# Performance work log

Measured on AMD Instinct MI355X. Metric: run time of the kernel, lower is better.

The kernel has to match this reference:

```python
import jax, jax.numpy as jnp
import numpy as np


def setup_inputs() -> dict:
    key = jax.random.key(0)
    ks = jax.random.split(key, 5)
    B, D, W = 8, 768, 128
    scale = 1.0 / np.sqrt(D)
    return {
        "x": jax.random.normal(ks[0], (B, D, W, W), dtype=jnp.float32),
        "in_proj_w": jax.random.normal(ks[1], (3 * D, D), dtype=jnp.float32) * scale,
        "in_proj_b": jax.random.normal(ks[2], (3 * D,), dtype=jnp.float32) * 0.01,
        "out_w": jax.random.normal(ks[3], (D, D), dtype=jnp.float32) * scale,
        "out_b": jax.random.normal(ks[4], (D,), dtype=jnp.float32) * 0.01,
        "num_heads": 12,
        "num_tokens": 8,
    }


def reference(x, in_proj_w, in_proj_b, out_w, out_b, num_heads, num_tokens):
    B, D, Wd, Hd = x.shape
    nt = num_tokens
    gs = Hd // nt            # grid (block) size
    T = nt * nt              # number of blocks / queries
    S = gs * gs              # k/v tokens per block
    h = num_heads
    hd = D // h

    # ---- query: adaptive avg pool to (nt, nt), flatten, permute -> (B, T, D)
    q = x.reshape(B, D, nt, gs, nt, gs).mean(axis=(3, 5))      # (B, D, nt, nt)
    q = q.reshape(B, D, T).transpose(0, 2, 1)                   # (B, T, D)

    # ---- key/value: faithful reproduction of unfold + view(x.size()) + reshape
    # torch: kv_perm (B,W,H,D) -> unfold -> (B, nt, nt, D, gs, gs) contiguous,
    # then reinterpreted flat as (B, W*H, D) (scrambles channel/pixel layout).
    t = x.transpose(0, 2, 3, 1)                                 # (B, W, H, D)
    t = t.reshape(B, nt, gs, nt, gs, D).transpose(0, 1, 3, 5, 2, 4)  # (B,nt,nt,D,gs,gs)
    kv = t.reshape(B, T, S, D)                                  # chunked into T blocks of S tokens

    # ---- in-projections (torch MultiheadAttention packed weights)
    Wq, Wk, Wv = in_proj_w[:D], in_proj_w[D:2 * D], in_proj_w[2 * D:]
    bq, bk, bv = in_proj_b[:D], in_proj_b[D:2 * D], in_proj_b[2 * D:]
    qp = (q @ Wq.T + bq).reshape(B, T, h, hd)                   # (B, T, h, hd)
    kp = (kv @ Wk.T + bk).reshape(B, T, S, h, hd)               # (B, T, S, h, hd)
    vp = (kv @ Wv.T + bv).reshape(B, T, S, h, hd)

    # ---- block-local single-query attention, batched over all T blocks
    scores = jnp.einsum("bthd,btshd->bths", qp, kp) / np.sqrt(hd)  # (B, T, h, S)
    attn = jax.nn.softmax(scores, axis=-1)
    ctx = jnp.einsum("bths,btshd->bthd", attn, vp).reshape(B, T, D)

    # ---- out projection
    return ctx @ out_w.T + out_b                                # (B, T, D)
```

## Files before the change

kernel.cpp:

```cpp
#include <hip/hip_runtime.h>
#include <hip/hip_bf16.h>

#define D_ 768
#define W_ 128
#define T_ 64
#define S_ 256
#define H_ 12
#define HH_ 6
#define BT_ 512

__device__ __forceinline__ unsigned short f2bf(float f) {
  unsigned u = __float_as_uint(f);
  u = (u + 0x7FFFu + ((u >> 16) & 1u)) >> 16;
  return (unsigned short)u;
}
__device__ __forceinline__ float bfu(unsigned s) {
  return __uint_as_float(s << 16);
}

__global__ __launch_bounds__(384) void k_pack(const float* __restrict__ x,
                                              unsigned short* __restrict__ packed,
                                              float* __restrict__ q) {
  const int blk  = blockIdx.x;
  const int cc   = blk & 15;
  const int tjp  = (blk >> 4) & 3;
  const int ti   = (blk >> 6) & 7;
  const int b    = blk >> 9;
  const int tid  = threadIdx.x;
  const int c8   = tid & 7;
  const int ch   = tid >> 3;
  const int btl  = c8 >> 2;
  const int btg0 = b*64 + ti*8 + tjp*2;
  const int ch0  = cc * 48;

  __shared__ unsigned short tile[48][2][260];
  __shared__ float poolsc[48][2];

  const float* xcol = x + (size_t)b*D_*16384 + (size_t)(ch0 + ch)*16384
                        + (16*ti)*128 + 32*tjp + c8*4;

  float psum = 0.f;
  #pragma unroll
  for (int r = 0; r < 16; ++r) {
    const float4 v = *(const float4*)(xcol + r*128);
    const int px = r*16 + (c8 & 3)*4;
    unsigned lo = (unsigned)f2bf(v.x) | ((unsigned)f2bf(v.y) << 16);
    unsigned hi = (unsigned)f2bf(v.z) | ((unsigned)f2bf(v.w) << 16);
    *(uint2*)&tile[ch][btl][px] = make_uint2(lo, hi);
    psum += (v.x + v.y) + (v.z + v.w);
  }
  psum += __shfl_xor(psum, 1);
  psum += __shfl_xor(psum, 2);
  if ((c8 & 3) == 0) poolsc[ch][btl] = psum;
  __syncthreads();

  for (int ii = tid; ii < 512; ii += 384) {
    const int bl = ii >> 8, p = ii & 255;
    unsigned short* pbt = packed + ((size_t)(btg0 + bl)*16 + cc)*D_*16;
    #pragma unroll
    for (int c = 0; c < 3; ++c) {
      unsigned u[8];
      #pragma unroll
      for (int k2 = 0; k2 < 8; ++k2) {
        const unsigned a  = tile[3*(2*k2)     + c][bl][p];
        const unsigned b2 = tile[3*(2*k2 + 1) + c][bl][p];
        u[k2] = a | (b2 << 16);
      }
      unsigned short* dst = pbt + (size_t)(c*256 + p)*16;
      *(uint4*)(dst)     = make_uint4(u[0], u[1], u[2], u[3]);
      *(uint4*)(dst + 8) = make_uint4(u[4], u[5], u[6], u[7]);
    }
  }
  if (tid < 96) {
    const int ch2 = tid >> 1, bl = tid & 1;
    q[(size_t)(btg0 + bl)*D_ + ch0 + ch2] = poolsc[ch2][bl] * (1.0f/256.0f);
  }
}

__global__ __launch_bounds__(256) void k_qp(const float* __restrict__ q,
                                            const float* __restrict__ ipw,
                                            const float* __restrict__ ipb,
                                            float* __restrict__ qp) {
  const int jt = blockIdx.x >> 6;
  const int bt0 = (blockIdx.x & 63) * 8;
  const int tid = threadIdx.x;
  const float* Wr = ipw + (size_t)jt*64*D_;
  __shared__ float wt[64][65];
  __shared__ float at[8][65];
  const int i = tid & 63, qw = tid >> 6;
  float acc[2] = {0,0};
  for (int dc = 0; dc < D_; dc += 64) {
    #pragma unroll
    for (int k = 0; k < 4; ++k) {
      const int idx = k*256 + tid;
      const int r = idx >> 4, c4 = idx & 15;
      *(float4*)&wt[r][c4*4] = *(const float4*)(Wr + (size_t)r*D_ + dc + c4*4);
    }
    if (tid < 128) {
      const int r = tid >> 4, c4 = tid & 15;
      *(float4*)&at[r][c4*4] = *(const float4*)(q + (size_t)(bt0 + r)*D_ + dc + c4*4);
    }
    __syncthreads();
    #pragma unroll
    for (int dd = 0; dd < 64; ++dd) {
      const float wv = wt[i][dd];
      #pragma unroll
      for (int k = 0; k < 2; ++k)
        acc[k] += at[qw + k*4][dd] * wv;
    }
    __syncthreads();
  }
  const float bqv = ipb[jt*64 + i];
  #pragma unroll
  for (int k = 0; k < 2; ++k)
    qp[(size_t)(bt0 + qw + k*4)*D_ + jt*64 + i] = acc[k] + bqv;
}

__global__ __launch_bounds__(256) void k_fold(const float* __restrict__ qp,
                                              const float* __restrict__ ipw,
                                              unsigned short* __restrict__ qkout) {
  const int btc = blockIdx.x & 15;
  const int nt  = blockIdx.x >> 4;
  const int h   = nt / 12;
  const int ddc = (nt % 12) * 64;
  const int bt0 = btc * 32;
  const int tid = threadIdx.x;
  __shared__ float qpl[32][68];
  __shared__ float wkl[64][68];
  #pragma unroll
  for (int k = 0; k < 2; ++k) {
    const int idx = k*256 + tid;
    const int r = idx >> 4, c4 = idx & 15;
    *(float4*)&qpl[r][c4*4] = *(const float4*)(qp + (size_t)(bt0 + r)*D_ + h*64 + c4*4);
  }
  #pragma unroll
  for (int k = 0; k < 4; ++k) {
    const int idx = k*256 + tid;
    const int r = idx >> 4, c4 = idx & 15;
    *(float4*)&wkl[r][c4*4] = *(const float4*)(ipw + (size_t)(D_ + h*64 + r)*D_ + ddc + c4*4);
  }
  __syncthreads();
  const int i = tid & 63, qw = tid >> 6;
  float acc[8] = {0,0,0,0,0,0,0,0};
  #pragma unroll 8
  for (int kk = 0; kk < 64; ++kk) {
    const float w = wkl[kk][i];
    #pragma unroll
    for (int k = 0; k < 8; ++k)
      acc[k] += qpl[qw + k*4][kk] * w;
  }
  #pragma unroll
  for (int k = 0; k < 8; ++k)
    qkout[((size_t)(bt0 + qw + k*4)*H_ + h)*D_ + ddc + i] = f2bf(acc[k] * 0.125f);
}

__global__ __launch_bounds__(256) void k_attn3(const unsigned short* __restrict__ packed,
                                               const unsigned short* __restrict__ qkin,
                                               unsigned short* __restrict__ wout) {
  const int bt = blockIdx.x >> 1;
  const int hg = blockIdx.x & 1;
  const int tid = threadIdx.x;
  const int wv = tid >> 6, lane = tid & 63;
  __shared__ float pool_lds[HH_ * D_];
  __shared__ float sc[HH_][S_];

  {
    const uint4* src = (const uint4*)(qkin + ((size_t)bt*H_ + hg*HH_)*D_);
    #pragma unroll
    for (int k = 0; k < 3; ++k) {
      const int idx = k*256 + tid;
      if (idx < 576) {
        const uint4 v = src[idx];
        float* d = pool_lds + idx*8;
        d[0] = bfu(v.x & 0xFFFFu); d[1] = bfu(v.x >> 16);
        d[2] = bfu(v.y & 0xFFFFu); d[3] = bfu(v.y >> 16);
        d[4] = bfu(v.z & 0xFFFFu); d[5] = bfu(v.z >> 16);
        d[6] = bfu(v.w & 0xFFFFu); d[7] = bfu(v.w >> 16);
      }
    }
  }
  __syncthreads();

  float acc[HH_][4];
  #pragma unroll
  for (int h = 0; h < HH_; ++h)
    #pragma unroll
    for (int j = 0; j < 4; ++j) acc[h][j] = 0.f;

  {
    const unsigned short* pb = packed + ((size_t)bt*16 + (lane >> 2))*D_*16 + (lane & 3)*4;
    const int d0 = wv * 192;
    short4 pv[4];
    #pragma unroll
    for (int dd = 0; dd < 4; ++dd)
      pv[dd] = *(const short4*)(pb + (size_t)(d0 + dd)*16);
    #pragma unroll 2
    for (int d4 = 0; d4 < 48; ++d4) {
      const int d = d0 + d4*4;
      short4 nx[4];
      if (d4 < 47) {
        #pragma unroll
        for (int dd = 0; dd < 4; ++dd)
          nx[dd] = *(const short4*)(pb + (size_t)(d + 4 + dd)*16);
      }
      float f[4][4];
      #pragma unroll
      for (int dd = 0; dd < 4; ++dd) {
        f[dd][0] = bfu((unsigned)(unsigned short)pv[dd].x);
        f[dd][1] = bfu((unsigned)(unsigned short)pv[dd].y);
        f[dd][2] = bfu((unsigned)(unsigned short)pv[dd].z);
        f[dd][3] = bfu((unsigned)(unsigned short)pv[dd].w);
      }
      #pragma unroll
      for (int h = 0; h < HH_; ++h) {
        const float4 qv = *(const float4*)&pool_lds[h*D_ + d];
        #pragma unroll
        for (int j = 0; j < 4; ++j)
          acc[h][j] += qv.x*f[0][j] + qv.y*f[1][j] + qv.z*f[2][j] + qv.w*f[3][j];
      }
      #pragma unroll
      for (int dd = 0; dd < 4; ++dd) pv[dd] = nx[dd];
    }
  }
  __syncthreads();

  if (wv == 0) {
    #pragma unroll
    for (int h = 0; h < HH_; ++h)
      *(float4*)&sc[h][lane*4] = make_float4(acc[h][0], acc[h][1], acc[h][2], acc[h][3]);
  } else {
    float* dstp = pool_lds + (size_t)(wv - 1)*(HH_*S_);
    #pragma unroll
    for (int h = 0; h < HH_; ++h)
      *(float4*)&dstp[h*S_ + lane*4] = make_float4(acc[h][0], acc[h][1], acc[h][2], acc[h][3]);
  }
  __syncthreads();
  #pragma unroll
  for (int h = 0; h < HH_; ++h)
    sc[h][tid] += pool_lds[0*(HH_*S_) + h*S_ + tid]
                + pool_lds[1*(HH_*S_) + h*S_ + tid]
                + pool_lds[2*(HH_*S_) + h*S_ + tid];
  __syncthreads();

  if (wv < 3) {
    #pragma unroll
    for (int hh = 0; hh < 2; ++hh) {
      const int h = wv*2 + hh;
      float4 v = *(const float4*)(&sc[h][lane*4]);
      float m = fmaxf(fmaxf(v.x, v.y), fmaxf(v.z, v.w));
      #pragma unroll
      for (int off = 32; off > 0; off >>= 1) m = fmaxf(m, __shfl_xor(m, off));
      const float e0 = __expf(v.x - m), e1 = __expf(v.y - m),
                  e2 = __expf(v.z - m), e3 = __expf(v.w - m);
      float ss = (e0+e1)+(e2+e3);
      #pragma unroll
      for (int off = 32; off > 0; off >>= 1) ss += __shfl_xor(ss, off);
      const float inv = 1.0f / ss;
      *(float4*)(&sc[h][lane*4]) = make_float4(e0*inv, e1*inv, e2*inv, e3*inv);
    }
  }
  __syncthreads();

  float wacc[HH_][3];
  #pragma unroll
  for (int h = 0; h < HH_; ++h) { wacc[h][0]=0.f; wacc[h][1]=0.f; wacc[h][2]=0.f; }
  const unsigned short* prow = packed + (size_t)bt*16*D_*16;
  uint4 pv3[3];
  #pragma unroll
  for (int c = 0; c < 3; ++c)
    pv3[c] = *(const uint4*)(prow + ((size_t)0*D_ + c*256 + tid)*16);
  #pragma unroll 2
  for (int s8 = 0; s8 < 32; ++s8) {
    uint4 nx3[3];
    if (s8 < 31) {
      const int t = s8 + 1;
      #pragma unroll
      for (int c = 0; c < 3; ++c)
        nx3[c] = *(const uint4*)(prow + ((size_t)(t >> 1)*D_ + c*256 + tid)*16 + (t & 1)*8);
    }
    float f[3][8];
    #pragma unroll
    for (int c = 0; c < 3; ++c) {
      f[c][0] = bfu(pv3[c].x & 0xFFFFu); f[c][1] = bfu(pv3[c].x >> 16);
      f[c][2] = bfu(pv3[c].y & 0xFFFFu); f[c][3] = bfu(pv3[c].y >> 16);
      f[c][4] = bfu(pv3[c].z & 0xFFFFu); f[c][5] = bfu(pv3[c].z >> 16);
      f[c][6] = bfu(pv3[c].w & 0xFFFFu); f[c][7] = bfu(pv3[c].w >> 16);
    }
    #pragma unroll
    for (int h = 0; h < HH_; ++h) {
      const float4 a0 = *(const float4*)&sc[h][s8*8];
      const float4 a1 = *(const float4*)&sc[h][s8*8 + 4];
      #pragma unroll
      for (int c = 0; c < 3; ++c)
        wacc[h][c] += a0.x*f[c][0] + a0.y*f[c][1] + a0.z*f[c][2] + a0.w*f[c][3]
                    + a1.x*f[c][4] + a1.y*f[c][5] + a1.z*f[c][6] + a1.w*f[c][7];
    }
    #pragma unroll
    for (int c = 0; c < 3; ++c) pv3[c] = nx3[c];
  }
  unsigned short* wp = wout + ((size_t)bt*H_ + hg*HH_)*D_;
  #pragma unroll
  for (int h = 0; h < HH_; ++h)
    #pragma unroll
    for (int c = 0; c < 3; ++c)
      wp[h*D_ + c*256 + tid] = f2bf(wacc[h][c]);
}

__global__ __launch_bounds__(256) void k_ctx(const unsigned short* __restrict__ wbuf,
                                             const float* __restrict__ ipw,
                                             const float* __restrict__ ipb,
                                             float* __restrict__ ctx) {
  const int h = blockIdx.x >> 6;
  const int bt0 = (blockIdx.x & 63) * 8;
  const int tid = threadIdx.x;
  const float* Wv = ipw + (size_t)2*D_*D_ + (size_t)h*64*D_;
  __shared__ float wt[64][65];
  __shared__ float at[8][65];
  const int i = tid & 63, qw = tid >> 6;
  float acc[2] = {0,0};
  for (int dc = 0; dc < D_; dc += 64) {
    #pragma unroll
    for (int k = 0; k < 4; ++k) {
      const int idx = k*256 + tid;
      const int r = idx >> 4, c4 = idx & 15;
      *(float4*)&wt[r][c4*4] = *(const float4*)(Wv + (size_t)r*D_ + dc + c4*4);
    }
    if (tid < 128) {
      const int r = tid >> 4, c4 = tid & 15;
      const uint2 v = *(const uint2*)(wbuf + ((size_t)(bt0 + r)*H_ + h)*D_ + dc + c4*4);
      at[r][c4*4 + 0] = bfu(v.x & 0xFFFFu);
      at[r][c4*4 + 1] = bfu(v.x >> 16);
      at[r][c4*4 + 2] = bfu(v.y & 0xFFFFu);
      at[r][c4*4 + 3] = bfu(v.y >> 16);
    }
    __syncthreads();
    #pragma unroll
    for (int dd = 0; dd < 64; ++dd) {
      const float wv = wt[i][dd];
      #pragma unroll
      for (int k = 0; k < 2; ++k)
        acc[k] += at[qw + k*4][dd] * wv;
    }
    __syncthreads();
  }
  const float bvv = ipb[2*D_ + h*64 + i];
  #pragma unroll
  for (int k = 0; k < 2; ++k)
    ctx[(size_t)(bt0 + qw + k*4)*D_ + h*64 + i] = acc[k] + bvv;
}

__global__ __launch_bounds__(256) void k_out(const float* __restrict__ ctx,
                                             const float* __restrict__ ow,
                                             const float* __restrict__ ob,
                                             float* __restrict__ out) {
  const int jt = blockIdx.x >> 6;
  const int bt0 = (blockIdx.x & 63) * 8;
  const int tid = threadIdx.x;
  const float* Wr = ow + (size_t)jt*64*D_;
  __shared__ float wt[64][65];
  __shared__ float at[8][65];
  const int i = tid & 63, qw = tid >> 6;
  float acc[2] = {0,0};
  for (int dc = 0; dc < D_; dc += 64) {
    #pragma unroll
    for (int k = 0; k < 4; ++k) {
      const int idx = k*256 + tid;
      const int r = idx >> 4, c4 = idx & 15;
      *(float4*)&wt[r][c4*4] = *(const float4*)(Wr + (size_t)r*D_ + dc + c4*4);
    }
    if (tid < 128) {
      const int r = tid >> 4, c4 = tid & 15;
      *(float4*)&at[r][c4*4] = *(const float4*)(ctx + (size_t)(bt0 + r)*D_ + dc + c4*4);
    }
    __syncthreads();
    #pragma unroll
    for (int dd = 0; dd < 64; ++dd) {
      const float wv = wt[i][dd];
      #pragma unroll
      for (int k = 0; k < 2; ++k)
        acc[k] += at[qw + k*4][dd] * wv;
    }
    __syncthreads();
  }
  const float obv = ob[jt*64 + i];
  #pragma unroll
  for (int k = 0; k < 2; ++k)
    out[(size_t)(bt0 + qw + k*4)*D_ + jt*64 + i] = acc[k] + obv;
}

__global__ __launch_bounds__(256) void k_q(const float* __restrict__ x, float* __restrict__ q) {
  const int bd = blockIdx.x;
  const int tid = threadIdx.x;
  const float4* xp = (const float4*)(x + (size_t)bd * (W_*W_));
  float acc[8] = {0,0,0,0,0,0,0,0};
  #pragma unroll
  for (int k = 0; k < 16; ++k) {
    float4 v = xp[k*256 + tid];
    acc[k>>1] += (v.x + v.y) + (v.z + v.w);
  }
  __shared__ float part[256][9];
  #pragma unroll
  for (int i = 0; i < 8; ++i) part[tid][i] = acc[i];
  __syncthreads();
  if (tid < 64) {
    const int ti = tid >> 3, tj = tid & 7;
    float s = 0.f;
    #pragma unroll
    for (int m = 0; m < 8; ++m)
      #pragma unroll
      for (int n = 0; n < 4; ++n)
        s += part[m*32 + tj*4 + n][ti];
    const int b = bd / D_, d = bd - b*D_;
    q[(size_t)(b*T_ + tid)*D_ + d] = s * (1.0f/256.0f);
  }
}

__global__ __launch_bounds__(256) void k_attn(const float* __restrict__ x,
                                              const unsigned short* __restrict__ qkin,
                                              unsigned short* __restrict__ wout) {
  const int bt = blockIdx.x;
  const int b = bt >> 6, t = bt & 63;
  const int ti = t >> 3, tj = t & 7;
  const int tid = threadIdx.x;
  __shared__ float qkl[H_*D_];
  __shared__ float sc[H_][S_];
  const float* xb = x + (size_t)b*D_*W_*W_ + ti*16*W_ + tj*16;
  {
    const uint4* src = (const uint4*)(qkin + (size_t)bt*H_*D_);
    #pragma unroll
    for (int k = 0; k < 5; ++k) {
      const int idx = k*256 + tid;
      if (idx < 1152) {
        const uint4 v = src[idx];
        float* d = qkl + idx*8;
        d[0] = bfu(v.x & 0xFFFFu); d[1] = bfu(v.x >> 16);
        d[2] = bfu(v.y & 0xFFFFu); d[3] = bfu(v.y >> 16);
        d[4] = bfu(v.z & 0xFFFFu); d[5] = bfu(v.z >> 16);
        d[6] = bfu(v.w & 0xFFFFu); d[7] = bfu(v.w >> 16);
      }
    }
  }
  __syncthreads();
  float acc[H_];
  #pragma unroll
  for (int h = 0; h < H_; ++h) acc[h] = 0.f;
  #pragma unroll
  for (int c = 0; c < 3; ++c) {
    const float* chp = xb + (size_t)(3*tid + c)*(W_*W_);
    for (int blk = 0; blk < 8; ++blk) {
      float4 v[8];
      #pragma unroll
      for (int u = 0; u < 8; ++u) {
        const int pg = blk*8 + u;
        v[u] = *(const float4*)(chp + (pg>>2)*W_ + (pg&3)*4);
      }
      const int dbase = c*256 + blk*32;
      #pragma unroll
      for (int h = 0; h < H_; ++h) {
        const float4* qh = (const float4*)(qkl + h*D_ + dbase);
        float s0 = 0.f;
        #pragma unroll
        for (int u = 0; u < 8; ++u) {
          const float4 qq = qh[u];
          s0 += qq.x*v[u].x + qq.y*v[u].y + qq.z*v[u].z + qq.w*v[u].w;
        }
        acc[h] += s0;
      }
    }
  }
  #pragma unroll
  for (int h = 0; h < H_; ++h) sc[h][tid] = acc[h];
  __syncthreads();
  {
    const int wv = tid >> 6, lane = tid & 63;
    #pragma unroll
    for (int hh = 0; hh < 3; ++hh) {
      const int h = wv*3 + hh;
      float4 v = *(const float4*)(&sc[h][lane*4]);
      float m = fmaxf(fmaxf(v.x, v.y), fmaxf(v.z, v.w));
      #pragma unroll
      for (int off = 32; off > 0; off >>= 1) m = fmaxf(m, __shfl_xor(m, off));
      const float e0 = __expf(v.x - m), e1 = __expf(v.y - m),
                  e2 = __expf(v.z - m), e3 = __expf(v.w - m);
      float ss = (e0+e1)+(e2+e3);
      #pragma unroll
      for (int off = 32; off > 0; off >>= 1) ss += __shfl_xor(ss, off);
      const float inv = 1.0f / ss;
      *(float4*)(&sc[h][lane*4]) = make_float4(e0*inv, e1*inv, e2*inv, e3*inv);
    }
  }
  __syncthreads();
  float wacc[H_][3];
  #pragma unroll
  for (int h = 0; h < H_; ++h) { wacc[h][0]=0.f; wacc[h][1]=0.f; wacc[h][2]=0.f; }
  const float* xp0 = xb + (tid>>4)*W_ + (tid&15);
  for (int s = 0; s < S_; ++s) {
    const float p0 = xp0[(size_t)(3*s+0)*(W_*W_)];
    const float p1 = xp0[(size_t)(3*s+1)*(W_*W_)];
    const float p2 = xp0[(size_t)(3*s+2)*(W_*W_)];
    #pragma unroll
    for (int h = 0; h < H_; ++h) {
      const float at = sc[h][s];
      wacc[h][0] += at*p0; wacc[h][1] += at*p1; wacc[h][2] += at*p2;
    }
  }
  unsigned short* wp = wout + (size_t)bt*H_*D_;
  #pragma unroll
  for (int h = 0; h < H_; ++h)
    #pragma unroll
    for (int c = 0; c < 3; ++c)
      wp[h*D_ + c*256 + tid] = f2bf(wacc[h][c]);
}

extern "C" void kernel_launch(void* const* d_in, const int* in_sizes, int n_in,
                              void* d_out, int out_size, void* d_ws, size_t ws_size,
                              hipStream_t stream) {
  const float* x   = (const float*)d_in[0];
  const float* ipw = (const float*)d_in[1];
  const float* ipb = (const float*)d_in[2];
  const float* ow  = (const float*)d_in[3];
  const float* ob  = (const float*)d_in[4];
  float* out = (float*)d_out;

  float* q    = (float*)d_ws;
  float* qp   = q    + (size_t)BT_*D_;
  unsigned short* qk = (unsigned short*)(qp + (size_t)BT_*D_);
  unsigned short* wb = (unsigned short*)(qp + (size_t)BT_*D_ + (size_t)BT_*H_*D_);
  float* ctxb = qp + (size_t)BT_*D_ + (size_t)BT_*H_*D_*2;
  unsigned short* packed = (unsigned short*)(ctxb + (size_t)BT_*D_);

  const size_t need_main = ((size_t)BT_*D_*3 + (size_t)BT_*H_*D_*2) * 4
                         + (size_t)BT_*D_*S_*2;

  if (ws_size >= need_main) {
    k_pack <<<dim3(4096), dim3(384), 0, stream>>>(x, packed, q);
    k_qp   <<<dim3(768),  dim3(256), 0, stream>>>(q, ipw, ipb, qp);
    k_fold <<<dim3(2304), dim3(256), 0, stream>>>(qp, ipw, qk);
    k_attn3<<<dim3(1024), dim3(256), 0, stream>>>(packed, qk, wb);
    k_ctx  <<<dim3(768),  dim3(256), 0, stream>>>(wb, ipw, ipb, ctxb);
    k_out  <<<dim3(768),  dim3(256), 0, stream>>>(ctxb, ow, ob, out);
  } else {
    k_q    <<<dim3(8*D_), dim3(256), 0, stream>>>(x, q);
    k_qp   <<<dim3(768),  dim3(256), 0, stream>>>(q, ipw, ipb, qp);
    k_fold <<<dim3(2304), dim3(256), 0, stream>>>(qp, ipw, qk);
    k_attn <<<dim3(BT_),  dim3(256), 0, stream>>>(x, qk, wb);
    k_ctx  <<<dim3(768),  dim3(256), 0, stream>>>(wb, ipw, ipb, ctxb);
    k_out  <<<dim3(768),  dim3(256), 0, stream>>>(ctxb, ow, ob, out);
  }
}
```

Measured before the change: 383.3 us.

## Use bf16 MFMA for attention scores and switch packed layout to token-major rows

```diff
diff --git a/kernel.cpp b/kernel.cpp
--- a/kernel.cpp
+++ b/kernel.cpp
@@ -6,8 +6,10 @@
 #define T_ 64
 #define S_ 256
 #define H_ 12
-#define HH_ 6
 #define BT_ 512
+
+typedef __attribute__((ext_vector_type(8))) short short8v;
+typedef __attribute__((ext_vector_type(4))) float f32x4;
 
 __device__ __forceinline__ unsigned short f2bf(float f) {
   unsigned u = __float_as_uint(f);
@@ -33,7 +35,7 @@
   const int btg0 = b*64 + ti*8 + tjp*2;
   const int ch0  = cc * 48;
 
-  __shared__ unsigned short tile[48][2][260];
+  __shared__ unsigned short tile[48][2][264];
   __shared__ float poolsc[48][2];
 
   const float* xcol = x + (size_t)b*D_*16384 + (size_t)(ch0 + ch)*16384
@@ -54,22 +56,18 @@
   if ((c8 & 3) == 0) poolsc[ch][btl] = psum;
   __syncthreads();
 
-  for (int ii = tid; ii < 512; ii += 384) {
-    const int bl = ii >> 8, p = ii & 255;
-    unsigned short* pbt = packed + ((size_t)(btg0 + bl)*16 + cc)*D_*16;
-    #pragma unroll
-    for (int c = 0; c < 3; ++c) {
-      unsigned u[8];
-      #pragma unroll
-      for (int k2 = 0; k2 < 8; ++k2) {
-        const unsigned a  = tile[3*(2*k2)     + c][bl][p];
-        const unsigned b2 = tile[3*(2*k2 + 1) + c][bl][p];
-        u[k2] = a | (b2 << 16);
-      }
-      unsigned short* dst = pbt + (size_t)(c*256 + p)*16;
-      *(uint4*)(dst)     = make_uint4(u[0], u[1], u[2], u[3]);
-      *(uint4*)(dst + 8) = make_uint4(u[4], u[5], u[6], u[7]);
-    }
+  for (int ii = tid; ii < 3072; ii += 384) {
+    const int btl2 = ii / 1536;
+    const int r2   = ii - btl2*1536;
+    const int sl   = r2 / 96;
+    const int r3   = r2 - sl*96;
+    const int c    = r3 >> 5;
+    const int p8   = r3 & 31;
+    const int chs  = sl*3 + c;
+    const uint4 v = *(const uint4*)&tile[chs][btl2][p8*8];
+    unsigned short* dst = packed + (size_t)(btg0 + btl2)*(S_*D_)
+                        + (size_t)(cc*16 + sl)*D_ + c*256 + p8*8;
+    *(uint4*)dst = v;
   }
   if (tid < 96) {
     const int ch2 = tid >> 1, bl = tid & 1;
@@ -154,98 +152,47 @@
     qkout[((size_t)(bt0 + qw + k*4)*H_ + h)*D_ + ddc + i] = f2bf(acc[k] * 0.125f);
 }
 
-__global__ __launch_bounds__(256) void k_attn3(const unsigned short* __restrict__ packed,
+__global__ __launch_bounds__(512) void k_attn4(const unsigned short* __restrict__ packed,
                                                const unsigned short* __restrict__ qkin,
                                                unsigned short* __restrict__ wout) {
-  const int bt = blockIdx.x >> 1;
-  const int hg = blockIdx.x & 1;
+  const int bt = blockIdx.x;
   const int tid = threadIdx.x;
   const int wv = tid >> 6, lane = tid & 63;
-  __shared__ float pool_lds[HH_ * D_];
-  __shared__ float sc[HH_][S_];
+  __shared__ float sc[12][260];
+
+  const int m16 = lane & 15;
+  const int kg  = lane >> 4;
+  const unsigned short* pbase = packed + (size_t)bt * (S_*D_);
 
   {
-    const uint4* src = (const uint4*)(qkin + ((size_t)bt*H_ + hg*HH_)*D_);
-    #pragma unroll
-    for (int k = 0; k < 3; ++k) {
-      const int idx = k*256 + tid;
-      if (idx < 576) {
-        const uint4 v = src[idx];
-        float* d = pool_lds + idx*8;
-        d[0] = bfu(v.x & 0xFFFFu); d[1] = bfu(v.x >> 16);
-        d[2] = bfu(v.y & 0xFFFFu); d[3] = bfu(v.y >> 16);
-        d[4] = bfu(v.z & 0xFFFFu); d[5] = bfu(v.z >> 16);
-        d[6] = bfu(v.w & 0xFFFFu); d[7] = bfu(v.w >> 16);
+    const int hB = (m16 < 12) ? m16 : 0;
+    const unsigned short* qb  = qkin + ((size_t)bt*H_ + hB)*D_ + kg*8;
+    const unsigned short* pA0 = pbase + (size_t)(wv*32      + m16)*D_ + kg*8;
+    const unsigned short* pA1 = pbase + (size_t)(wv*32 + 16 + m16)*D_ + kg*8;
+    f32x4 acc0 = {0.f,0.f,0.f,0.f};
+    f32x4 acc1 = {0.f,0.f,0.f,0.f};
+    #pragma unroll 4
+    for (int ks = 0; ks < 24; ++ks) {
+      const short8v b  = *(const short8v*)(qb  + ks*32);
+      const short8v a0 = *(const short8v*)(pA0 + ks*32);
+      const short8v a1 = *(const short8v*)(pA1 + ks*32);
+      acc0 = __builtin_amdgcn_mfma_f32_16x16x32_bf16(a0, b, acc0, 0, 0, 0);
+      acc1 = __builtin_amdgcn_mfma_f32_16x16x32_bf16(a1, b, acc1, 0, 0, 0);
+    }
+    if (m16 < 12) {
+      #pragma unroll
+      for (int r = 0; r < 4; ++r) {
+        sc[m16][wv*32      + kg*4 + r] = acc0[r];
+        sc[m16][wv*32 + 16 + kg*4 + r] = acc1[r];
       }
     }
   }
   __syncthreads();
 
-  float acc[HH_][4];
-  #pragma unroll
-  for (int h = 0; h < HH_; ++h)
-    #pragma unroll
-    for (int j = 0; j < 4; ++j) acc[h][j] = 0.f;
-
-  {
-    const unsigned short* pb = packed + ((size_t)bt*16 + (lane >> 2))*D_*16 + (lane & 3)*4;
-    const int d0 = wv * 192;
-    short4 pv[4];
-    #pragma unroll
-    for (int dd = 0; dd < 4; ++dd)
-      pv[dd] = *(const short4*)(pb + (size_t)(d0 + dd)*16);
-    #pragma unroll 2
-    for (int d4 = 0; d4 < 48; ++d4) {
-      const int d = d0 + d4*4;
-      short4 nx[4];
-      if (d4 < 47) {
-        #pragma unroll
-        for (int dd = 0; dd < 4; ++dd)
-          nx[dd] = *(const short4*)(pb + (size_t)(d + 4 + dd)*16);
-      }
-      float f[4][4];
-      #pragma unroll
-      for (int dd = 0; dd < 4; ++dd) {
-        f[dd][0] = bfu((unsigned)(unsigned short)pv[dd].x);
-        f[dd][1] = bfu((unsigned)(unsigned short)pv[dd].y);
-        f[dd][2] = bfu((unsigned)(unsigned short)pv[dd].z);
-        f[dd][3] = bfu((unsigned)(unsigned short)pv[dd].w);
-      }
-      #pragma unroll
-      for (int h = 0; h < HH_; ++h) {
-        const float4 qv = *(const float4*)&pool_lds[h*D_ + d];
-        #pragma unroll
-        for (int j = 0; j < 4; ++j)
-          acc[h][j] += qv.x*f[0][j] + qv.y*f[1][j] + qv.z*f[2][j] + qv.w*f[3][j];
-      }
-      #pragma unroll
-      for (int dd = 0; dd < 4; ++dd) pv[dd] = nx[dd];
-    }
-  }
-  __syncthreads();
-
-  if (wv == 0) {
-    #pragma unroll
-    for (int h = 0; h < HH_; ++h)
-      *(float4*)&sc[h][lane*4] = make_float4(acc[h][0], acc[h][1], acc[h][2], acc[h][3]);
-  } else {
-    float* dstp = pool_lds + (size_t)(wv - 1)*(HH_*S_);
-    #pragma unroll
-    for (int h = 0; h < HH_; ++h)
-      *(float4*)&dstp[h*S_ + lane*4] = make_float4(acc[h][0], acc[h][1], acc[h][2], acc[h][3]);
-  }
-  __syncthreads();
-  #pragma unroll
-  for (int h = 0; h < HH_; ++h)
-    sc[h][tid] += pool_lds[0*(HH_*S_) + h*S_ + tid]
-                + pool_lds[1*(HH_*S_) + h*S_ + tid]
-                + pool_lds[2*(HH_*S_) + h*S_ + tid];
-  __syncthreads();
-
-  if (wv < 3) {
-    #pragma unroll
-    for (int hh = 0; hh < 2; ++hh) {
-      const int h = wv*2 + hh;
+  #pragma unroll
+  for (int pass = 0; pass < 2; ++pass) {
+    if (pass == 0 || wv < 4) {
+      const int h = (pass == 0) ? wv : 8 + wv;
       float4 v = *(const float4*)(&sc[h][lane*4]);
       float m = fmaxf(fmaxf(v.x, v.y), fmaxf(v.z, v.w));
       #pragma unroll
@@ -261,49 +208,47 @@
   }
   __syncthreads();
 
-  float wacc[HH_][3];
-  #pragma unroll
-  for (int h = 0; h < HH_; ++h) { wacc[h][0]=0.f; wacc[h][1]=0.f; wacc[h][2]=0.f; }
-  const unsigned short* prow = packed + (size_t)bt*16*D_*16;
-  uint4 pv3[3];
-  #pragma unroll
-  for (int c = 0; c < 3; ++c)
-    pv3[c] = *(const uint4*)(prow + ((size_t)0*D_ + c*256 + tid)*16);
-  #pragma unroll 2
-  for (int s8 = 0; s8 < 32; ++s8) {
-    uint4 nx3[3];
-    if (s8 < 31) {
-      const int t = s8 + 1;
-      #pragma unroll
-      for (int c = 0; c < 3; ++c)
-        nx3[c] = *(const uint4*)(prow + ((size_t)(t >> 1)*D_ + c*256 + tid)*16 + (t & 1)*8);
-    }
-    float f[3][8];
-    #pragma unroll
-    for (int c = 0; c < 3; ++c) {
-      f[c][0] = bfu(pv3[c].x & 0xFFFFu); f[c][1] = bfu(pv3[c].x >> 16);
-      f[c][2] = bfu(pv3[c].y & 0xFFFFu); f[c][3] = bfu(pv3[c].y >> 16);
-      f[c][4] = bfu(pv3[c].z & 0xFFFFu); f[c][5] = bfu(pv3[c].z >> 16);
-      f[c][6] = bfu(pv3[c].w & 0xFFFFu); f[c][7] = bfu(pv3[c].w >> 16);
-    }
-    #pragma unroll
-    for (int h = 0; h < HH_; ++h) {
-      const float4 a0 = *(const float4*)&sc[h][s8*8];
-      const float4 a1 = *(const float4*)&sc[h][s8*8 + 4];
-      #pragma unroll
-      for (int c = 0; c < 3; ++c)
-        wacc[h][c] += a0.x*f[c][0] + a0.y*f[c][1] + a0.z*f[c][2] + a0.w*f[c][3]
-                    + a1.x*f[c][4] + a1.y*f[c][5] + a1.z*f[c][6] + a1.w*f[c][7];
-    }
-    #pragma unroll
-    for (int c = 0; c < 3; ++c) pv3[c] = nx3[c];
-  }
-  unsigned short* wp = wout + ((size_t)bt*H_ + hg*HH_)*D_;
-  #pragma unroll
-  for (int h = 0; h < HH_; ++h)
-    #pragma unroll
-    for (int c = 0; c < 3; ++c)
-      wp[h*D_ + c*256 + tid] = f2bf(wacc[h][c]);
+  if (tid < 384) {
+    const int hb  = (tid / 96) * 3;
+    const int dd8 = (tid - (hb/3)*96) * 8;
+    float wacc[3][8];
+    #pragma unroll
+    for (int hh = 0; hh < 3; ++hh)
+      #pragma unroll
+      for (int j = 0; j < 8; ++j) wacc[hh][j] = 0.f;
+    const unsigned short* pr = pbase + dd8;
+    uint4 cur = *(const uint4*)pr;
+    #pragma unroll 2
+    for (int s = 0; s < 256; ++s) {
+      uint4 nx = make_uint4(0,0,0,0);
+      if (s < 255) nx = *(const uint4*)(pr + (size_t)(s + 1)*D_);
+      float f[8];
+      f[0] = bfu(cur.x & 0xFFFFu); f[1] = bfu(cur.x >> 16);
+      f[2] = bfu(cur.y & 0xFFFFu); f[3] = bfu(cur.y >> 16);
+      f[4] = bfu(cur.z & 0xFFFFu); f[5] = bfu(cur.z >> 16);
+      f[6] = bfu(cur.w & 0xFFFFu); f[7] = bfu(cur.w >> 16);
+      const float a0 = sc[hb + 0][s];
+      const float a1 = sc[hb + 1][s];
+      const float a2 = sc[hb + 2][s];
+      #pragma unroll
+      for (int j = 0; j < 8; ++j) {
+        wacc[0][j] += a0 * f[j];
+        wacc[1][j] += a1 * f[j];
+        wacc[2][j] += a2 * f[j];
+      }
+      cur = nx;
+    }
+    unsigned short* wp = wout + ((size_t)bt*H_ + hb)*D_ + dd8;
+    #pragma unroll
+    for (int hh = 0; hh < 3; ++hh) {
+      uint4 o;
+      o.x = (unsigned)f2bf(wacc[hh][0]) | ((unsigned)f2bf(wacc[hh][1]) << 16);
+      o.y = (unsigned)f2bf(wacc[hh][2]) | ((unsigned)f2bf(wacc[hh][3]) << 16);
+      o.z = (unsigned)f2bf(wacc[hh][4]) | ((unsigned)f2bf(wacc[hh][5]) << 16);
+      o.w = (unsigned)f2bf(wacc[hh][6]) | ((unsigned)f2bf(wacc[hh][7]) << 16);
+      *(uint4*)(wp + (size_t)hh*D_) = o;
+    }
+  }
 }
 
 __global__ __launch_bounds__(256) void k_ctx(const unsigned short* __restrict__ wbuf,
@@ -536,7 +481,7 @@
     k_pack <<<dim3(4096), dim3(384), 0, stream>>>(x, packed, q);
     k_qp   <<<dim3(768),  dim3(256), 0, stream>>>(q, ipw, ipb, qp);
     k_fold <<<dim3(2304), dim3(256), 0, stream>>>(qp, ipw, qk);
-    k_attn3<<<dim3(1024), dim3(256), 0, stream>>>(packed, qk, wb);
+    k_attn4<<<dim3(BT_),  dim3(512), 0, stream>>>(packed, qk, wb);
     k_ctx  <<<dim3(768),  dim3(256), 0, stream>>>(wb, ipw, ipb, ctxb);
     k_out  <<<dim3(768),  dim3(256), 0, stream>>>(ctxb, ow, ob, out);
   } else {
```

New measurement: 342.8 us (median of 2 runs). -10.6%, faster.
